# Kernel tuning notes

Hardware: AMD Instinct MI355X
Metric: run time of the kernel (lower is better)

Reference implementation:

```python
import jax, jax.numpy as jnp
import numpy as np

N = 10000   # num_nodes
F = 64      # latent_dim
U = 128     # num_units
B = 8       # batch
K = 2       # gcn_step
E = 160000  # edges (avg degree 16)
M = 2 * K + 1  # num_matrices = len(supports)*gcn_step + 1


def setup_inputs() -> dict:
    rng = np.random.default_rng(0)
    rows = rng.integers(0, N, E).astype(np.int32)
    cols = rng.integers(0, N, E).astype(np.int32)
    vals = (rng.random(E).astype(np.float32) + 0.1)
    # random-walk normalization D^{-1} A, per the original utils.calculate_random_walk_matrix
    deg_out = np.zeros(N, np.float32); np.add.at(deg_out, rows, vals)
    deg_in = np.zeros(N, np.float32); np.add.at(deg_in, cols, vals)
    # support1 = (D_out^{-1} A)^T : out[c] += vals/d_out[r] * x[r]  -> dst=cols, src=rows
    w1 = vals / np.maximum(deg_out[rows], 1e-8)
    # support2 = (D_in^{-1} A^T)^T : out[r] += vals/d_in[c] * x[c]  -> dst=rows, src=cols
    w2 = vals / np.maximum(deg_in[cols], 1e-8)

    key = jax.random.key(0)
    ks = jax.random.split(key, 4)

    def xavier(k, shape):
        std = (2.0 / (shape[0] + shape[1])) ** 0.5
        return jax.random.normal(k, shape, jnp.float32) * std

    return {
        'y': jax.random.normal(ks[0], (B, N * F), jnp.float32),
        'W_lat': xavier(ks[1], (M * F, F)),
        'b_lat': jnp.ones((F,), jnp.float32),   # bias_start=1.0, shared (keyed by length)
        'W_units': xavier(ks[2], (M * F, U)),
        'b_units': jnp.zeros((U,), jnp.float32),
        'W_final': xavier(ks[3], (M * U, F)),
        'sup1_w': jnp.asarray(w1),
        'sup2_w': jnp.asarray(w2),
        'edge_rows': jnp.asarray(rows),
        'edge_cols': jnp.asarray(cols),
    }


def _spmm(dst, src, w, x):
    # sparse matmul S @ x with S given as COO edge list; x: (N, Fin, B)
    return jax.ops.segment_sum(w[:, None, None] * x[src], dst, num_segments=N)


def _gconv(x, supports, W, b):
    # x: (B, N, Fin) -> (B, N*Fout); Chebyshev diffusion convolution
    Bsz, n, fin = x.shape
    x0 = jnp.transpose(x, (1, 2, 0))  # (N, Fin, B)
    xs = [x0]
    for dst, src, w in supports:
        xk_2 = x0
        x1 = _spmm(dst, src, w, x0)
        xs.append(x1)
        for _ in range(2, K + 1):
            x2 = 2.0 * _spmm(dst, src, w, x1) - xk_2
            xs.append(x2)
            xk_2, x1 = x1, x2
    X = jnp.stack(xs, axis=-1)                       # (N, Fin, B, M)
    X = jnp.transpose(X, (2, 0, 1, 3)).reshape(Bsz * n, fin * len(xs))  # feature-major, matrix-minor
    out = X @ W + b
    return out.reshape(Bsz, n * W.shape[1])


def reference(y, W_lat, b_lat, W_units, b_units, W_final, sup1_w, sup2_w, edge_rows, edge_cols):
    supports = [(edge_cols, edge_rows, sup1_w), (edge_rows, edge_cols, sup2_w)]
    x = y.reshape(B, N, F)
    # theta gate (bias_start=1.0 via shared b_lat)
    theta = jax.nn.sigmoid(_gconv(x, supports, W_lat, b_lat))
    # ode_func_net: gen_layers=1 hidden gconv + final gconv (final bias is shared b_lat!)
    c = jnp.tanh(_gconv(x, supports, W_units, b_units)).reshape(B, N, U)
    c = jnp.tanh(_gconv(c, supports, W_final, b_lat))
    return -theta * c
```

## Files before the change

kernel.cpp:

```cpp
#include <hip/hip_runtime.h>

#define N_NODES 10000
#define NEDGE 160000
#define NB 80000
#define EPAD (NEDGE + 8 * N_NODES)

typedef unsigned int u32;
typedef unsigned short u16;
typedef __attribute__((ext_vector_type(8))) short short8;
typedef __attribute__((ext_vector_type(4))) float float4v;

__device__ __forceinline__ u16 f2bf(float f) {
    u32 u = __float_as_uint(f);
    return (u16)((u + 0x7fffu + ((u >> 16) & 1u)) >> 16);
}
__device__ __forceinline__ float lo16(u32 u) { return __uint_as_float(u << 16); }
__device__ __forceinline__ float hi16(u32 u) { return __uint_as_float(u & 0xffff0000u); }
__device__ __forceinline__ u32 pack2(float a, float b) {
    return (u32)f2bf(a) | (((u32)f2bf(b)) << 16);
}
__device__ __forceinline__ float fast_tanh(float v) {
    return 1.f - 2.f / (__expf(2.f * v) + 1.f);
}

static const size_t SLAB = (size_t)NB * 64;

__global__ __launch_bounds__(256) void prepcount_kernel(
    const float2* __restrict__ y, u32* __restrict__ X0,
    const float* __restrict__ W_lat, const float* __restrict__ W_units,
    u16* __restrict__ bpk12, const float* __restrict__ W_final, u16* __restrict__ bpkP,
    const int* __restrict__ rows, const int* __restrict__ cols, int* __restrict__ cnt) {
    int b = blockIdx.x, t = threadIdx.x;
    if (b < 10000) {
        int idx = b * 256 + t;
        int fh = idx & 31;
        int rb = idx >> 5;
        int bb = rb & 7;
        int n = rb >> 3;
        float2 v = y[((size_t)bb * N_NODES + n) * 32 + fh];
        X0[idx] = pack2(v.x, v.y);
    } else if (b < 10240) {
        int idx = (b - 10000) * 256 + t;
        int j = idx & 7;
        int lane = (idx >> 3) & 63;
        int rest = idx >> 9;
        int ct = rest % 12;
        int ks = rest / 12;
        int k = ks * 32 + (lane >> 4) * 8 + j;
        int col = ct * 16 + (lane & 15);
        int wrow = (k % 64) * 5 + (k / 64);
        float v = (col < 64) ? W_lat[wrow * 64 + col] : W_units[wrow * 128 + (col - 64)];
        bpk12[idx] = f2bf(v);
    } else if (b < 10400) {
        int idx = (b - 10240) * 256 + t;
        int j8 = idx & 7;
        int lane = (idx >> 3) & 63;
        int rest = idx >> 9;
        int ct = rest % 20;
        int ks = rest / 20;
        int k = ks * 32 + (lane >> 4) * 8 + j8;
        int col = ct * 16 + (lane & 15);
        int slot = col >> 6, j = col & 63;
        float v;
        if (slot == 0)
            v = W_final[(k * 5 + 0) * 64 + j] - W_final[(k * 5 + 2) * 64 + j] -
                W_final[(k * 5 + 4) * 64 + j];
        else
            v = W_final[(k * 5 + slot) * 64 + j];
        bpkP[idx] = f2bf(v);
    } else {
        int e = (b - 10400) * 256 + t;
        atomicAdd(&cnt[cols[e]], 1);
        atomicAdd(&cnt[N_NODES + rows[e]], 1);
    }
}

__global__ void blocksum_kernel(const int* __restrict__ cnt, int* __restrict__ bsums) {
    __shared__ int red[4];
    int arr = blockIdx.x / 40;
    int c = blockIdx.x % 40;
    int idx = c * 256 + threadIdx.x;
    int v = (idx < N_NODES) ? ((cnt[arr * N_NODES + idx] + 7) & ~7) : 0;
#pragma unroll
    for (int off = 32; off; off >>= 1) v += __shfl_down(v, off, 64);
    int wv = threadIdx.x >> 6, ln = threadIdx.x & 63;
    if (ln == 0) red[wv] = v;
    __syncthreads();
    if (threadIdx.x == 0) bsums[blockIdx.x] = red[0] + red[1] + red[2] + red[3];
}

__global__ void scanapply_kernel(int* __restrict__ cnt, const int* __restrict__ bsums,
                                 int* __restrict__ rowptr1, int* __restrict__ rowptr2) {
    __shared__ int lds[256];
    int arr = blockIdx.x / 40;
    int c = blockIdx.x % 40;
    int base = 0;
    for (int i = 0; i < c; i++) base += bsums[arr * 40 + i];
    int idx = c * 256 + threadIdx.x;
    bool ok = idx < N_NODES;
    int v = ok ? ((cnt[arr * N_NODES + idx] + 7) & ~7) : 0;
    int t = threadIdx.x;
    lds[t] = v;
    __syncthreads();
    for (int off = 1; off < 256; off <<= 1) {
        int add = (t >= off) ? lds[t - off] : 0;
        __syncthreads();
        lds[t] += add;
        __syncthreads();
    }
    int excl = lds[t] - v + base;
    if (ok) {
        int* rp = arr ? rowptr2 : rowptr1;
        rp[idx] = excl;
        cnt[arr * N_NODES + idx] = excl;
    }
    if (c == 39 && t == 255) {
        (arr ? rowptr2 : rowptr1)[N_NODES] = base + lds[255];
    }
}

__global__ void scatter_kernel(const int* __restrict__ rows, const int* __restrict__ cols,
                               const float* __restrict__ w1, const float* __restrict__ w2,
                               int* __restrict__ cur1, int* __restrict__ cur2,
                               int2* __restrict__ edges1, int2* __restrict__ edges2) {
    int e = blockIdx.x * 256 + threadIdx.x;
    if (e < NEDGE) {
        int r = rows[e], c = cols[e];
        int p1 = atomicAdd(&cur1[c], 1);
        edges1[p1] = make_int2(r, __float_as_int(w1[e]));
        int p2 = atomicAdd(&cur2[r], 1);
        edges2[p2] = make_int2(c, __float_as_int(w2[e]));
    }
}

__device__ __forceinline__ void gacc(float* acc, float w, uint4 u) {
    acc[0] += w * lo16(u.x); acc[1] += w * hi16(u.x);
    acc[2] += w * lo16(u.y); acc[3] += w * hi16(u.y);
    acc[4] += w * lo16(u.z); acc[5] += w * hi16(u.z);
    acc[6] += w * lo16(u.w); acc[7] += w * hi16(u.w);
}

__device__ __forceinline__ void gather_sliced(const u32* __restrict__ Xin,
                                              const int* __restrict__ rp,
                                              const int2* __restrict__ eg,
                                              int row, bool valid, int su, int l,
                                              float* acc) {
    int e = 0, e1 = 0;
    if (valid) {
        e = rp[row] + l;
        e1 = rp[row + 1];
    }
    while (__ballot(e < e1)) {
        int2 me = make_int2(0, 0);
        if (e < e1) me = eg[e];
#pragma unroll
        for (int j = 0; j < 8; j++) {
            int s = __shfl(me.x, j, 8);
            float w = __int_as_float(__shfl(me.y, j, 8));
            uint4 u = *(const uint4*)(Xin + (size_t)s * 256 + su + l * 4);
            gacc(acc, w, u);
        }
        e += 8;
    }
}

__global__ __launch_bounds__(256) void spmm2_kernel(
    const u32* __restrict__ XinA, const u32* __restrict__ XprevA, u32* __restrict__ XoutA,
    const u32* __restrict__ XinB, const u32* __restrict__ XprevB, u32* __restrict__ XoutB,
    const int* __restrict__ rowptr1, const int2* __restrict__ edges1,
    const int* __restrict__ rowptr2, const int2* __restrict__ edges2,
    float alpha, float beta) {
    int t = threadIdx.x;
    int lane = t & 63;
    int g = lane >> 3, l = lane & 7;
    int slice = blockIdx.x & 7;
    int chunk = blockIdx.x >> 3;
    int su = slice * 32;
    int v = chunk * 32 + (t >> 6) * 8 + g;
    bool hB = v >= N_NODES;
    int n = hB ? v - N_NODES : v;
    const u32* Xin = hB ? XinB : XinA;
    const u32* Xprev = hB ? XprevB : XprevA;
    u32* Xout = hB ? XoutB : XoutA;
    const int* rp = hB ? rowptr2 : rowptr1;
    const int2* eg = hB ? edges2 : edges1;

    float acc[8] = {0.f, 0.f, 0.f, 0.f, 0.f, 0.f, 0.f, 0.f};
    gather_sliced(Xin, rp, eg, n, true, su, l, acc);

    size_t o = (size_t)n * 256 + su + l * 4;
    if (beta != 0.f) {
        uint4 p = *(const uint4*)(Xprev + o);
        acc[0] = alpha * acc[0] + beta * lo16(p.x); acc[1] = alpha * acc[1] + beta * hi16(p.x);
        acc[2] = alpha * acc[2] + beta * lo16(p.y); acc[3] = alpha * acc[3] + beta * hi16(p.y);
        acc[4] = alpha * acc[4] + beta * lo16(p.z); acc[5] = alpha * acc[5] + beta * hi16(p.z);
        acc[6] = alpha * acc[6] + beta * lo16(p.w); acc[7] = alpha * acc[7] + beta * hi16(p.w);
    } else {
#pragma unroll
        for (int i = 0; i < 8; i++) acc[i] *= alpha;
    }
    uint4 r;
    r.x = pack2(acc[0], acc[1]);
    r.y = pack2(acc[2], acc[3]);
    r.z = pack2(acc[4], acc[5]);
    r.w = pack2(acc[6], acc[7]);
    *(uint4*)(Xout + o) = r;
}

__global__ __launch_bounds__(256) void spmm_final_kernel(
    const u32* __restrict__ T1, const u32* __restrict__ T2,
    const u32* __restrict__ Q, const u32* __restrict__ theta,
    const int* __restrict__ rowptr1, const int2* __restrict__ edges1,
    const int* __restrict__ rowptr2, const int2* __restrict__ edges2,
    float* __restrict__ outF) {
    int t = threadIdx.x;
    int lane = t & 63;
    int g = lane >> 3, l = lane & 7;
    int slice = blockIdx.x & 7;
    int chunk = blockIdx.x >> 3;
    int su = slice * 32;
    int n = chunk * 32 + (t >> 6) * 8 + g;
    bool valid = n < N_NODES;

    float acc[8] = {0.f, 0.f, 0.f, 0.f, 0.f, 0.f, 0.f, 0.f};
    gather_sliced(T1, rowptr1, edges1, n, valid, su, l, acc);
    gather_sliced(T2, rowptr2, edges2, n, valid, su, l, acc);
    if (!valid) return;

    size_t o = (size_t)n * 256 + su + l * 4;
    uint4 q = *(const uint4*)(Q + o);
    uint4 th = *(const uint4*)(theta + o);
    float res[8];
    res[0] = -lo16(th.x) * fast_tanh(lo16(q.x) + acc[0]);
    res[1] = -hi16(th.x) * fast_tanh(hi16(q.x) + acc[1]);
    res[2] = -lo16(th.y) * fast_tanh(lo16(q.y) + acc[2]);
    res[3] = -hi16(th.y) * fast_tanh(hi16(q.y) + acc[3]);
    res[4] = -lo16(th.z) * fast_tanh(lo16(q.z) + acc[4]);
    res[5] = -hi16(th.z) * fast_tanh(hi16(q.z) + acc[5]);
    res[6] = -lo16(th.w) * fast_tanh(lo16(q.w) + acc[6]);
    res[7] = -hi16(th.w) * fast_tanh(hi16(q.w) + acc[7]);
    float* dst = outF + (size_t)slice * (N_NODES * 64) + (size_t)n * 64 + l * 8;
    *(float4*)(dst) = make_float4(res[0], res[1], res[2], res[3]);
    *(float4*)(dst + 4) = make_float4(res[4], res[5], res[6], res[7]);
}

struct Slabs { const u16* p[5]; };

template <int FIN, int NM, int NOUT, int NSPLIT, int MODE>
__global__ __launch_bounds__(320) void gemm_kernel(
    Slabs A, const u16* __restrict__ Bp, const float* __restrict__ bias1,
    const float* __restrict__ bias2, u16* __restrict__ O1, u16* __restrict__ O2) {
    constexpr int K = NM * FIN;
    constexpr int KS = K / 32;
    constexpr int CTT = NOUT / 16;
    constexpr int CT = CTT / NSPLIT;
    __shared__ u16 Blds[KS * CT * 64 * 8];

    int t = threadIdx.x;
    int lane = t & 63;
    int wave = t >> 6;
    int slice = blockIdx.x & 7;
    int rest = blockIdx.x >> 3;
    int nodeG = rest / NSPLIT;
    int half = rest % NSPLIT;
    int ctBase = half * CT;
    int mrow = lane & 15;
    int kq = lane >> 4;
    int node0 = nodeG * 80 + wave * 16;

    for (int idx = t; idx < KS * CT * 64; idx += 320) {
        int bl = idx & 63;
        int ct = (idx >> 6) % CT;
        int ks = idx / (64 * CT);
        *(uint4*)(Blds + (size_t)idx * 8) =
            *(const uint4*)(Bp + ((size_t)(ks * CTT + ctBase + ct) * 64 + bl) * 8);
    }
    __syncthreads();

    float4v acc[CT];
#pragma unroll
    for (int c = 0; c < CT; c++) acc[c] = (float4v){0.f, 0.f, 0.f, 0.f};

    size_t r = (size_t)(node0 + mrow) * 8 + slice;
#pragma unroll
    for (int ks = 0; ks < KS; ks++) {
        int k = ks * 32 + kq * 8;
        int m = k / FIN;
        int koff = k % FIN;
        short8 a = *(const short8*)(A.p[m] + r * FIN + koff);
#pragma unroll
        for (int ct = 0; ct < CT; ct++) {
            short8 b = *(const short8*)(Blds + ((size_t)(ks * CT + ct) * 64 + lane) * 8);
            acc[ct] = __builtin_amdgcn_mfma_f32_16x16x32_bf16(b, a, acc[ct], 0, 0, 0);
        }
    }

#pragma unroll
    for (int ct = 0; ct < CT; ct++) {
        int col0 = (ctBase + ct) * 16 + kq * 4;
        float v[4];
#pragma unroll
        for (int i = 0; i < 4; i++) v[i] = acc[ct][i];
        if (MODE == 0) {
            if (col0 < 64) {
#pragma unroll
                for (int i = 0; i < 4; i++) v[i] += bias1[col0 + i];
            }
            uint2 w = make_uint2(pack2(v[0], v[1]), pack2(v[2], v[3]));
            u16* dst = O1 + (size_t)(col0 >> 6) * SLAB + r * 64 + (col0 & 63);
            *(uint2*)dst = w;
        } else {
            if (col0 < 64) {
#pragma unroll
                for (int i = 0; i < 4; i++)
                    v[i] = 1.f / (1.f + __expf(-(v[i] + bias1[col0 + i])));
                uint2 w = make_uint2(pack2(v[0], v[1]), pack2(v[2], v[3]));
                *(uint2*)(O1 + r * 64 + col0) = w;
            } else {
#pragma unroll
                for (int i = 0; i < 4; i++)
                    v[i] = fast_tanh(v[i] + bias2[col0 - 64 + i]);
                uint2 w = make_uint2(pack2(v[0], v[1]), pack2(v[2], v[3]));
                *(uint2*)(O2 + r * 128 + (col0 - 64)) = w;
            }
        }
    }
}

extern "C" void kernel_launch(void* const* d_in, const int* in_sizes, int n_in,
                              void* d_out, int out_size, void* d_ws, size_t ws_size,
                              hipStream_t stream) {
    const float2* y    = (const float2*)d_in[0];
    const float* W_lat = (const float*)d_in[1];
    const float* b_lat = (const float*)d_in[2];
    const float* W_units = (const float*)d_in[3];
    const float* b_units = (const float*)d_in[4];
    const float* W_final = (const float*)d_in[5];
    const float* sup1w = (const float*)d_in[6];
    const float* sup2w = (const float*)d_in[7];
    const int* rows    = (const int*)d_in[8];
    const int* cols    = (const int*)d_in[9];
    float* out = (float*)d_out;

    char* ws = (char*)d_ws;
    size_t off = 0;
    auto alloc = [&](size_t bytes) -> void* {
        void* p = ws + off;
        off += (bytes + 511) & ~(size_t)511;
        return p;
    };
    int* rowptr1 = (int*)alloc((N_NODES + 1) * 4);
    int* rowptr2 = (int*)alloc((N_NODES + 1) * 4);
    int* cnt = (int*)alloc((size_t)2 * N_NODES * 4);
    int* bsums = (int*)alloc(80 * 4);
    int2* edges1 = (int2*)alloc((size_t)EPAD * 8);
    int2* edges2 = (int2*)alloc((size_t)EPAD * 8);
    u16* bpk12 = (u16*)alloc((size_t)61440 * 2);
    u16* bpkP = (u16*)alloc((size_t)40960 * 2);
    u16* theta = (u16*)alloc((size_t)NB * 64 * 2);
    u16* S = (u16*)alloc((size_t)5 * NB * 64 * 2);
    u16* H0 = (u16*)alloc((size_t)NB * 128 * 2);
    u16* T1 = (u16*)alloc((size_t)NB * 64 * 2);
    u16* T2 = (u16*)alloc((size_t)NB * 64 * 2);

    hipMemsetAsync(cnt, 0, (size_t)2 * N_NODES * 4, stream);
    hipMemsetAsync(edges1, 0, (size_t)EPAD * 8, stream);
    hipMemsetAsync(edges2, 0, (size_t)EPAD * 8, stream);
    prepcount_kernel<<<11025, 256, 0, stream>>>(y, (u32*)S, W_lat, W_units, bpk12,
                                                W_final, bpkP, rows, cols, cnt);
    blocksum_kernel<<<80, 256, 0, stream>>>(cnt, bsums);
    scanapply_kernel<<<80, 256, 0, stream>>>(cnt, bsums, rowptr1, rowptr2);
    scatter_kernel<<<625, 256, 0, stream>>>(rows, cols, sup1w, sup2w,
                                            cnt, cnt + N_NODES, edges1, edges2);

    const u32* S0 = (const u32*)S;
    u32* X1 = (u32*)(S + 1 * SLAB);
    u32* X2 = (u32*)(S + 2 * SLAB);
    u32* X3 = (u32*)(S + 3 * SLAB);
    u32* X4 = (u32*)(S + 4 * SLAB);
    spmm2_kernel<<<5000, 256, 0, stream>>>(S0, nullptr, X1, S0, nullptr, X3,
                                           rowptr1, edges1, rowptr2, edges2, 1.f, 0.f);
    spmm2_kernel<<<5000, 256, 0, stream>>>(X1, S0, X2, X3, S0, X4,
                                           rowptr1, edges1, rowptr2, edges2, 2.f, -1.f);

    Slabs SX;
    for (int m = 0; m < 5; m++) SX.p[m] = S + (size_t)m * SLAB;
    gemm_kernel<64, 5, 192, 2, 1><<<2000, 320, 0, stream>>>(SX, bpk12, b_lat, b_units, theta, H0);

    Slabs SH;
    SH.p[0] = H0;
    gemm_kernel<128, 1, 320, 2, 0><<<2000, 320, 0, stream>>>(SH, bpkP, b_lat, nullptr, S, nullptr);

    const u32* Q  = (const u32*)(S + 0 * SLAB);
    const u32* P1 = (const u32*)(S + 1 * SLAB);
    const u32* P2 = (const u32*)(S + 2 * SLAB);
    const u32* P3 = (const u32*)(S + 3 * SLAB);
    const u32* P4 = (const u32*)(S + 4 * SLAB);
    spmm2_kernel<<<5000, 256, 0, stream>>>(P2, P1, (u32*)T1, P4, P3, (u32*)T2,
                                           rowptr1, edges1, rowptr2, edges2, 2.f, 1.f);
    spmm_final_kernel<<<2504, 256, 0, stream>>>((const u32*)T1, (const u32*)T2, Q,
                                                (const u32*)theta,
                                                rowptr1, edges1, rowptr2, edges2, out);
}
```

Baseline: 334.9 us.

## Restructure GEMM tiling: waves split output columns, B read directly from global

The two dense GEMM kernels now give each 256-thread block 32 contiguous rows, and each of its 4 waves owns a quarter of the output column tiles. Each wave computes two 16-row MFMA tiles so every B fragment is reused twice. The LDS staging of the packed weights and its barrier are removed, so B fragments are read straight from global memory and served by cache. The row indexing changes from node-major with a slice interleave to flat rows, and launch bounds now request higher occupancy. In exchange, every wave re-reads B from cache and the A rows are loaded once per wave, so four times per block.

```diff
diff --git a/kernel.cpp b/kernel.cpp
--- a/kernel.cpp
+++ b/kernel.cpp
@@ -246,82 +246,78 @@
 
 struct Slabs { const u16* p[5]; };
 
-template <int FIN, int NM, int NOUT, int NSPLIT, int MODE>
-__global__ __launch_bounds__(320) void gemm_kernel(
+template <int FIN, int NM, int NOUT, int CT, int MODE>
+__global__ __launch_bounds__(256, 6) void gemm_kernel(
     Slabs A, const u16* __restrict__ Bp, const float* __restrict__ bias1,
     const float* __restrict__ bias2, u16* __restrict__ O1, u16* __restrict__ O2) {
     constexpr int K = NM * FIN;
     constexpr int KS = K / 32;
     constexpr int CTT = NOUT / 16;
-    constexpr int CT = CTT / NSPLIT;
-    __shared__ u16 Blds[KS * CT * 64 * 8];
+    static_assert(CT * 4 == CTT, "4 waves cover all col tiles");
 
     int t = threadIdx.x;
     int lane = t & 63;
     int wave = t >> 6;
-    int slice = blockIdx.x & 7;
-    int rest = blockIdx.x >> 3;
-    int nodeG = rest / NSPLIT;
-    int half = rest % NSPLIT;
-    int ctBase = half * CT;
+    int ctBase = wave * CT;
+    int rowBase = blockIdx.x * 32;
     int mrow = lane & 15;
     int kq = lane >> 4;
-    int node0 = nodeG * 80 + wave * 16;
-
-    for (int idx = t; idx < KS * CT * 64; idx += 320) {
-        int bl = idx & 63;
-        int ct = (idx >> 6) % CT;
-        int ks = idx / (64 * CT);
-        *(uint4*)(Blds + (size_t)idx * 8) =
-            *(const uint4*)(Bp + ((size_t)(ks * CTT + ctBase + ct) * 64 + bl) * 8);
-    }
-    __syncthreads();
-
-    float4v acc[CT];
-#pragma unroll
-    for (int c = 0; c < CT; c++) acc[c] = (float4v){0.f, 0.f, 0.f, 0.f};
-
-    size_t r = (size_t)(node0 + mrow) * 8 + slice;
+
+    float4v acc0[CT], acc1[CT];
+#pragma unroll
+    for (int c = 0; c < CT; c++) {
+        acc0[c] = (float4v){0.f, 0.f, 0.f, 0.f};
+        acc1[c] = (float4v){0.f, 0.f, 0.f, 0.f};
+    }
+
 #pragma unroll
     for (int ks = 0; ks < KS; ks++) {
         int k = ks * 32 + kq * 8;
         int m = k / FIN;
         int koff = k % FIN;
-        short8 a = *(const short8*)(A.p[m] + r * FIN + koff);
+        const u16* ap = A.p[m];
+        short8 a0 = *(const short8*)(ap + (size_t)(rowBase + mrow) * FIN + koff);
+        short8 a1 = *(const short8*)(ap + (size_t)(rowBase + 16 + mrow) * FIN + koff);
 #pragma unroll
         for (int ct = 0; ct < CT; ct++) {
-            short8 b = *(const short8*)(Blds + ((size_t)(ks * CT + ct) * 64 + lane) * 8);
-            acc[ct] = __builtin_amdgcn_mfma_f32_16x16x32_bf16(b, a, acc[ct], 0, 0, 0);
+            short8 b = *(const short8*)(Bp +
+                        ((size_t)(ks * CTT + ctBase + ct) * 64 + lane) * 8);
+            acc0[ct] = __builtin_amdgcn_mfma_f32_16x16x32_bf16(b, a0, acc0[ct], 0, 0, 0);
+            acc1[ct] = __builtin_amdgcn_mfma_f32_16x16x32_bf16(b, a1, acc1[ct], 0, 0, 0);
         }
     }
 
 #pragma unroll
-    for (int ct = 0; ct < CT; ct++) {
-        int col0 = (ctBase + ct) * 16 + kq * 4;
-        float v[4];
-#pragma unroll
-        for (int i = 0; i < 4; i++) v[i] = acc[ct][i];
-        if (MODE == 0) {
-            if (col0 < 64) {
-#pragma unroll
-                for (int i = 0; i < 4; i++) v[i] += bias1[col0 + i];
-            }
-            uint2 w = make_uint2(pack2(v[0], v[1]), pack2(v[2], v[3]));
-            u16* dst = O1 + (size_t)(col0 >> 6) * SLAB + r * 64 + (col0 & 63);
-            *(uint2*)dst = w;
-        } else {
-            if (col0 < 64) {
-#pragma unroll
-                for (int i = 0; i < 4; i++)
-                    v[i] = 1.f / (1.f + __expf(-(v[i] + bias1[col0 + i])));
+    for (int hr = 0; hr < 2; hr++) {
+        size_t r = (size_t)(rowBase + hr * 16 + mrow);
+#pragma unroll
+        for (int ct = 0; ct < CT; ct++) {
+            float4v av = hr ? acc1[ct] : acc0[ct];
+            int col0 = (ctBase + ct) * 16 + kq * 4;
+            float v[4];
+#pragma unroll
+            for (int i = 0; i < 4; i++) v[i] = av[i];
+            if (MODE == 0) {
+                if (col0 < 64) {
+#pragma unroll
+                    for (int i = 0; i < 4; i++) v[i] += bias1[col0 + i];
+                }
                 uint2 w = make_uint2(pack2(v[0], v[1]), pack2(v[2], v[3]));
-                *(uint2*)(O1 + r * 64 + col0) = w;
+                *(uint2*)(O1 + (size_t)(col0 >> 6) * SLAB + r * 64 + (col0 & 63)) = w;
             } else {
-#pragma unroll
-                for (int i = 0; i < 4; i++)
-                    v[i] = fast_tanh(v[i] + bias2[col0 - 64 + i]);
-                uint2 w = make_uint2(pack2(v[0], v[1]), pack2(v[2], v[3]));
-                *(uint2*)(O2 + r * 128 + (col0 - 64)) = w;
+                if (col0 < 64) {
+#pragma unroll
+                    for (int i = 0; i < 4; i++)
+                        v[i] = 1.f / (1.f + __expf(-(v[i] + bias1[col0 + i])));
+                    uint2 w = make_uint2(pack2(v[0], v[1]), pack2(v[2], v[3]));
+                    *(uint2*)(O1 + r * 64 + col0) = w;
+                } else {
+#pragma unroll
+                    for (int i = 0; i < 4; i++)
+                        v[i] = fast_tanh(v[i] + bias2[col0 - 64 + i]);
+                    uint2 w = make_uint2(pack2(v[0], v[1]), pack2(v[2], v[3]));
+                    *(uint2*)(O2 + r * 128 + (col0 - 64)) = w;
+                }
             }
         }
     }
@@ -385,11 +381,11 @@
 
     Slabs SX;
     for (int m = 0; m < 5; m++) SX.p[m] = S + (size_t)m * SLAB;
-    gemm_kernel<64, 5, 192, 2, 1><<<2000, 320, 0, stream>>>(SX, bpk12, b_lat, b_units, theta, H0);
+    gemm_kernel<64, 5, 192, 3, 1><<<2500, 256, 0, stream>>>(SX, bpk12, b_lat, b_units, theta, H0);
 
     Slabs SH;
     SH.p[0] = H0;
-    gemm_kernel<128, 1, 320, 2, 0><<<2000, 320, 0, stream>>>(SH, bpkP, b_lat, nullptr, S, nullptr);
+    gemm_kernel<128, 1, 320, 5, 0><<<2500, 256, 0, stream>>>(SH, bpkP, b_lat, nullptr, S, nullptr);
 
     const u32* Q  = (const u32*)(S + 0 * SLAB);
     const u32* P1 = (const u32*)(S + 1 * SLAB);
```

After: 334.7 us. About the same (-0.0%).

## Switch activation slabs to batch-major layout and load GEMM weights directly

Applied to the files above, without the earlier changes.

Changes the bf16 activation layout from node-interleaved (node*256 + batch slice) to batch-major contiguous slabs (batch*320000 + node*32), which makes the input pack a straight copy and gives each spmm slice a contiguous region. The GEMM drops its LDS staging of the packed weights and reads B fragments straight from global memory, relying on cache. The first GEMM also goes from two column splits to one with half the blocks. The intent is to improve gather locality per batch slice and cut LDS and sync overhead, at the cost of more global and L2 weight traffic and fewer blocks.

```diff
diff --git a/kernel.cpp b/kernel.cpp
--- a/kernel.cpp
+++ b/kernel.cpp
@@ -32,13 +32,11 @@
     const int* __restrict__ rows, const int* __restrict__ cols, int* __restrict__ cnt) {
     int b = blockIdx.x, t = threadIdx.x;
     if (b < 10000) {
-        int idx = b * 256 + t;
-        int fh = idx & 31;
-        int rb = idx >> 5;
-        int bb = rb & 7;
-        int n = rb >> 3;
-        float2 v = y[((size_t)bb * N_NODES + n) * 32 + fh];
-        X0[idx] = pack2(v.x, v.y);
+        int batch = b & 7;
+        int chunk = b >> 3;
+        size_t base = (size_t)batch * 320000 + (size_t)chunk * 256;
+        float2 v = y[base + t];
+        X0[base + t] = pack2(v.x, v.y);
     } else if (b < 10240) {
         int idx = (b - 10000) * 256 + t;
         int j = idx & 7;
@@ -143,7 +141,7 @@
 __device__ __forceinline__ void gather_sliced(const u32* __restrict__ Xin,
                                               const int* __restrict__ rp,
                                               const int2* __restrict__ eg,
-                                              int row, bool valid, int su, int l,
+                                              int row, bool valid, size_t sbase, int l,
                                               float* acc) {
     int e = 0, e1 = 0;
     if (valid) {
@@ -157,7 +155,7 @@
         for (int j = 0; j < 8; j++) {
             int s = __shfl(me.x, j, 8);
             float w = __int_as_float(__shfl(me.y, j, 8));
-            uint4 u = *(const uint4*)(Xin + (size_t)s * 256 + su + l * 4);
+            uint4 u = *(const uint4*)(Xin + sbase + (size_t)s * 32 + l * 4);
             gacc(acc, w, u);
         }
         e += 8;
@@ -175,7 +173,7 @@
     int g = lane >> 3, l = lane & 7;
     int slice = blockIdx.x & 7;
     int chunk = blockIdx.x >> 3;
-    int su = slice * 32;
+    size_t sbase = (size_t)slice * 320000;
     int v = chunk * 32 + (t >> 6) * 8 + g;
     bool hB = v >= N_NODES;
     int n = hB ? v - N_NODES : v;
@@ -186,9 +184,9 @@
     const int2* eg = hB ? edges2 : edges1;
 
     float acc[8] = {0.f, 0.f, 0.f, 0.f, 0.f, 0.f, 0.f, 0.f};
-    gather_sliced(Xin, rp, eg, n, true, su, l, acc);
-
-    size_t o = (size_t)n * 256 + su + l * 4;
+    gather_sliced(Xin, rp, eg, n, true, sbase, l, acc);
+
+    size_t o = sbase + (size_t)n * 32 + l * 4;
     if (beta != 0.f) {
         uint4 p = *(const uint4*)(Xprev + o);
         acc[0] = alpha * acc[0] + beta * lo16(p.x); acc[1] = alpha * acc[1] + beta * hi16(p.x);
@@ -218,16 +216,16 @@
     int g = lane >> 3, l = lane & 7;
     int slice = blockIdx.x & 7;
     int chunk = blockIdx.x >> 3;
-    int su = slice * 32;
+    size_t sbase = (size_t)slice * 320000;
     int n = chunk * 32 + (t >> 6) * 8 + g;
     bool valid = n < N_NODES;
 
     float acc[8] = {0.f, 0.f, 0.f, 0.f, 0.f, 0.f, 0.f, 0.f};
-    gather_sliced(T1, rowptr1, edges1, n, valid, su, l, acc);
-    gather_sliced(T2, rowptr2, edges2, n, valid, su, l, acc);
+    gather_sliced(T1, rowptr1, edges1, n, valid, sbase, l, acc);
+    gather_sliced(T2, rowptr2, edges2, n, valid, sbase, l, acc);
     if (!valid) return;
 
-    size_t o = (size_t)n * 256 + su + l * 4;
+    size_t o = sbase + (size_t)n * 32 + l * 4;
     uint4 q = *(const uint4*)(Q + o);
     uint4 th = *(const uint4*)(theta + o);
     float res[8];
@@ -254,47 +252,38 @@
     constexpr int KS = K / 32;
     constexpr int CTT = NOUT / 16;
     constexpr int CT = CTT / NSPLIT;
-    __shared__ u16 Blds[KS * CT * 64 * 8];
 
     int t = threadIdx.x;
     int lane = t & 63;
     int wave = t >> 6;
-    int slice = blockIdx.x & 7;
+    int batch = blockIdx.x & 7;
     int rest = blockIdx.x >> 3;
-    int nodeG = rest / NSPLIT;
-    int half = rest % NSPLIT;
+    int nodeG = rest % 125;
+    int half = rest / 125;
     int ctBase = half * CT;
+    size_t rowBase = (size_t)batch * 10000 + nodeG * 80 + wave * 16;
     int mrow = lane & 15;
     int kq = lane >> 4;
-    int node0 = nodeG * 80 + wave * 16;
-
-    for (int idx = t; idx < KS * CT * 64; idx += 320) {
-        int bl = idx & 63;
-        int ct = (idx >> 6) % CT;
-        int ks = idx / (64 * CT);
-        *(uint4*)(Blds + (size_t)idx * 8) =
-            *(const uint4*)(Bp + ((size_t)(ks * CTT + ctBase + ct) * 64 + bl) * 8);
-    }
-    __syncthreads();
 
     float4v acc[CT];
 #pragma unroll
     for (int c = 0; c < CT; c++) acc[c] = (float4v){0.f, 0.f, 0.f, 0.f};
 
-    size_t r = (size_t)(node0 + mrow) * 8 + slice;
 #pragma unroll
     for (int ks = 0; ks < KS; ks++) {
         int k = ks * 32 + kq * 8;
         int m = k / FIN;
         int koff = k % FIN;
-        short8 a = *(const short8*)(A.p[m] + r * FIN + koff);
+        short8 a = *(const short8*)(A.p[m] + (rowBase + mrow) * FIN + koff);
 #pragma unroll
         for (int ct = 0; ct < CT; ct++) {
-            short8 b = *(const short8*)(Blds + ((size_t)(ks * CT + ct) * 64 + lane) * 8);
+            short8 b = *(const short8*)(Bp +
+                        ((size_t)(ks * CTT + ctBase + ct) * 64 + lane) * 8);
             acc[ct] = __builtin_amdgcn_mfma_f32_16x16x32_bf16(b, a, acc[ct], 0, 0, 0);
         }
     }
 
+    size_t r = rowBase + mrow;
 #pragma unroll
     for (int ct = 0; ct < CT; ct++) {
         int col0 = (ctBase + ct) * 16 + kq * 4;
@@ -307,8 +296,7 @@
                 for (int i = 0; i < 4; i++) v[i] += bias1[col0 + i];
             }
             uint2 w = make_uint2(pack2(v[0], v[1]), pack2(v[2], v[3]));
-            u16* dst = O1 + (size_t)(col0 >> 6) * SLAB + r * 64 + (col0 & 63);
-            *(uint2*)dst = w;
+            *(uint2*)(O1 + (size_t)(col0 >> 6) * SLAB + r * 64 + (col0 & 63)) = w;
         } else {
             if (col0 < 64) {
 #pragma unroll
@@ -385,7 +373,7 @@
 
     Slabs SX;
     for (int m = 0; m < 5; m++) SX.p[m] = S + (size_t)m * SLAB;
-    gemm_kernel<64, 5, 192, 2, 1><<<2000, 320, 0, stream>>>(SX, bpk12, b_lat, b_units, theta, H0);
+    gemm_kernel<64, 5, 192, 1, 1><<<1000, 320, 0, stream>>>(SX, bpk12, b_lat, b_units, theta, H0);
 
     Slabs SH;
     SH.p[0] = H0;
```

Measured after the change: 329.3 us. Within noise of the previous version (-1.7%).
